# Optimization experiments

Measured on AMD Instinct MI355X. Metric: run time of the kernel, lower is better.

Reference implementation:

```python
import jax, jax.numpy as jnp
import numpy as np

C = 256
RED = 8
CR = C // RED  # 32
B, H, W = 4, 64, 64
EPS = 1e-5


def setup_inputs() -> dict:
    key = jax.random.key(0)
    ks = jax.random.split(key, 12)
    s = 0.05
    return {
        "x": jax.random.normal(ks[0], (B, C, H, W), dtype=jnp.float32),
        "Wq": jax.random.normal(ks[1], (CR, C), dtype=jnp.float32) * s,
        "bq": jax.random.normal(ks[2], (CR,), dtype=jnp.float32) * s,
        "Wk": jax.random.normal(ks[3], (CR, C), dtype=jnp.float32) * s,
        "bk": jax.random.normal(ks[4], (CR,), dtype=jnp.float32) * s,
        "Wv": jax.random.normal(ks[5], (C, C), dtype=jnp.float32) * s,
        "bv": jax.random.normal(ks[6], (C,), dtype=jnp.float32) * s,
        "Wo": jax.random.normal(ks[7], (C, C), dtype=jnp.float32) * s,
        "bo": jax.random.normal(ks[8], (C,), dtype=jnp.float32) * s,
        "gamma": jnp.ones((C,), dtype=jnp.float32),
        "beta": jnp.zeros((C,), dtype=jnp.float32),
        "running_mean": jax.random.normal(ks[9], (C,), dtype=jnp.float32) * s,
        "running_var": jax.random.uniform(ks[10], (C,), dtype=jnp.float32, minval=0.5, maxval=1.5),
    }


def reference(x, Wq, bq, Wk, bk, Wv, bv, Wo, bo, gamma, beta, running_mean, running_var):
    b, c, h, w = x.shape
    n = h * w
    scale = c ** (-0.5)  # use_scale=True: in_channels**-0.5
    xf = x.reshape(b, c, n)  # [B, C, N]
    # 1x1 convs == per-pixel channel matmuls
    q = jnp.einsum('oc,bcn->bon', Wq, xf) + bq[None, :, None]   # [B, CR, N]
    k = jnp.einsum('oc,bcn->bon', Wk, xf) + bk[None, :, None]   # [B, CR, N]
    v = jnp.einsum('oc,bcn->bon', Wv, xf) + bv[None, :, None]   # [B, C, N]
    # attention[b, q_pos, k_pos], softmax over key positions (dim=2)
    attn = jnp.einsum('bcq,bck->bqk', q, k) * scale             # [B, N, N]
    attn = jax.nn.softmax(attn, axis=2)
    # out[b, c, q_pos] = sum_k v[b, c, k] * attn[b, q_pos, k]
    out = jnp.einsum('bck,bqk->bcq', v, attn)                   # [B, C, N]
    out = jnp.einsum('oc,bcn->bon', Wo, out) + bo[None, :, None]
    # BatchNorm2d (inference: running stats)
    inv = gamma / jnp.sqrt(running_var + EPS)
    out = out * inv[None, :, None] + (beta - running_mean * inv)[None, :, None]
    out = out.reshape(b, c, h, w)
    return jax.nn.relu(out + x)
```

## Files before the change

### kernel.cpp

```cpp
#include <hip/hip_runtime.h>
#include <hip/hip_bf16.h>

typedef unsigned short u16;
typedef unsigned int u32;

#define B_ 4
#define C_ 256
#define N_ 4096

constexpr float C1 = 0.09016844005556021f;

typedef float f32x16 __attribute__((ext_vector_type(16)));
typedef short bf16x8 __attribute__((ext_vector_type(8)));
typedef u32 u32x4 __attribute__((ext_vector_type(4)));
typedef int i32x2 __attribute__((ext_vector_type(2)));

__device__ __forceinline__ u16 bf16r(float f) {
    union { float f; u32 u; } a; a.f = f;
    u32 u = a.u;
    u += 0x7fffu + ((u >> 16) & 1u);
    return (u16)(u >> 16);
}

__device__ __forceinline__ float bf2f(u16 h) {
    union { u32 u; float f; } a; a.u = ((u32)h) << 16; return a.f;
}

__device__ __forceinline__ u32 pk2(float a, float b) {
    __hip_bfloat162 h = __float22bfloat162_rn(make_float2(a, b));
    union { __hip_bfloat162 h; u32 u; } c; c.h = h;
    return c.u;
}

__device__ __forceinline__ u32 cvtpk(float lo, float hi) {
    u32 r;
    asm("v_cvt_pk_bf16_f32 %0, %1, %2" : "=v"(r) : "v"(lo), "v"(hi));
    return r;
}

__device__ __forceinline__ void swap32(u32 &a, u32 &b) {
#if __has_builtin(__builtin_amdgcn_permlane32_swap)
    i32x2 r = __builtin_amdgcn_permlane32_swap((int)a, (int)b, false, false);
    a = (u32)r.x; b = (u32)r.y;
#else
    u32 as = __shfl_xor(a, 32), bs = __shfl_xor(b, 32);
    int hi = (threadIdx.x & 32) ? 1 : 0;
    u32 na = hi ? bs : a;
    u32 nb = hi ? b : as;
    a = na; b = nb;
#endif
}

__device__ __forceinline__ bf16x8 ld8(const u16* p) {
    return *reinterpret_cast<const bf16x8*>(p);
}

__device__ __forceinline__ void gld_lds16(const u16* g, u16* lbase, int lane) {
#if __has_builtin(__builtin_amdgcn_global_load_lds)
    __builtin_amdgcn_global_load_lds(
        (const __attribute__((address_space(1))) void*)g,
        (__attribute__((address_space(3))) void*)lbase, 16, 0, 0);
#else
    *reinterpret_cast<bf16x8*>(lbase + lane * 8) = ld8(g);
#endif
}

__device__ __forceinline__ int crow(int r, int hi) { return (r & 3) + 8 * (r >> 2) + 4 * hi; }

__global__ __launch_bounds__(256) void prep(
    const float* __restrict__ Wq, const float* __restrict__ Wk,
    const float* __restrict__ Wv, const float* __restrict__ Wo,
    const float* __restrict__ bo, const float* __restrict__ gamma,
    const float* __restrict__ beta, const float* __restrict__ rm, const float* __restrict__ rv,
    u16* __restrict__ wqk, u16* __restrict__ wv_b, u16* __restrict__ wo_b,
    float* __restrict__ scale, float* __restrict__ shift)
{
    int i = blockIdx.x * 256 + threadIdx.x;
    if (i < 16384) {
        float w = (i < 8192) ? Wq[i] * C1 : Wk[i - 8192];
        wqk[i] = bf16r(w);
    } else if (i < 81920) {
        wv_b[i - 16384] = bf16r(Wv[i - 16384]);
    } else if (i < 147456) {
        wo_b[i - 81920] = bf16r(Wo[i - 81920]);
    } else if (i < 147712) {
        int o = i - 147456;
        float inv = gamma[o] * rsqrtf(rv[o] + 1e-5f);
        scale[o] = inv;
        shift[o] = beta[o] + (bo[o] - rm[o]) * inv;
    }
}

__global__ __launch_bounds__(512) void projf(
    const float* __restrict__ x, const u16* __restrict__ wqk, const u16* __restrict__ wv,
    const float* __restrict__ bq, const float* __restrict__ bk, const float* __restrict__ bv,
    u16* __restrict__ qkt, u16* __restrict__ vout)
{
    __shared__ u16 xt[64 * 256];
    int tid = threadIdx.x;
    int lane = tid & 63, wid = tid >> 6;
    int r31 = lane & 31, hi = lane >> 5;
    int b = blockIdx.y, n0 = blockIdx.x * 64;
    const float* xb = x + (size_t)b * C_ * N_ + n0;
#pragma unroll
    for (int i = 0; i < 16; ++i) {
        int c2 = i * 8 + wid;
        int n = lane;
        float a0 = xb[(size_t)(2 * c2) * N_ + n];
        float a1 = xb[(size_t)(2 * c2 + 1) * N_ + n];
        int slot = (c2 >> 2) ^ (n & 31);
        *reinterpret_cast<u32*>(&xt[n * 256 + slot * 8 + (c2 & 3) * 2]) = pk2(a0, a1);
    }
    __syncthreads();
    for (int i = 0; i < 3; ++i) {
        int t = wid + i * 8;
        if (t < 20) {
            bool isqk = (t < 4);
            int nb = isqk ? (t >> 1) * 32 : ((t - 4) & 1) * 32;
            int gb = isqk ? (t & 1) * 32 : ((t - 4) >> 1) * 32;
            const u16* grow = (isqk ? wqk : wv) + (size_t)(gb + r31) * C_ + hi * 8;
            f32x16 acc;
#pragma unroll
            for (int r = 0; r < 16; ++r) acc[r] = 0.f;
#pragma unroll
            for (int ks = 0; ks < 16; ++ks) {
                int slot = (2 * ks + hi) ^ r31;
                bf16x8 lf = ld8(&xt[(nb + r31) * 256 + slot * 8]);
                bf16x8 gf = ld8(grow + ks * 16);
                if (isqk) acc = __builtin_amdgcn_mfma_f32_32x32x16_bf16(lf, gf, acc, 0, 0, 0);
                else      acc = __builtin_amdgcn_mfma_f32_32x32x16_bf16(gf, lf, acc, 0, 0, 0);
            }
            if (isqk) {
                int o = gb + r31;
                float bias = (o < 32) ? bq[o] * C1 : bk[o - 32];
                u16* qrow = qkt + ((size_t)b * N_ + n0 + nb) * 64 + o;
#pragma unroll
                for (int r = 0; r < 16; ++r)
                    qrow[(size_t)crow(r, hi) * 64] = bf16r(acc[r] + bias);
            } else {
                u16* vb = vout + (size_t)b * C_ * N_ + n0 + nb + r31;
#pragma unroll
                for (int r = 0; r < 16; ++r) {
                    int c = gb + crow(r, hi);
                    vb[(size_t)c * N_] = bf16r(acc[r] + bv[c]);
                }
            }
        }
    }
}

__global__ __launch_bounds__(256, 2) void attn(
    const u16* __restrict__ qkt, const u16* __restrict__ v,
    u16* __restrict__ opart, float* __restrict__ lpart, int kts)
{
    __shared__ char smem[73728];
    u16* vt0 = (u16*)smem;
    u16* kt0 = (u16*)(smem + 65536);
    int tid = threadIdx.x;
    int lane = tid & 63, wid = tid >> 6;
    int r31 = lane & 31, hi = lane >> 5;

    int nwg = 32 * 4 * gridDim.z;
    int wgl = blockIdx.x + 32 * (blockIdx.y + 4 * blockIdx.z);
    int cpx = nwg >> 3;
    int swzid = (wgl & 7) * cpx + (wgl >> 3);
    int bx = swzid & 31;
    int by = (swzid >> 5) & 3;
    int bz = swzid >> 7;

    int b = by, zs = bz;
    int q0 = bx * 128 + wid * 32;
    const u16* qkb = qkt + (size_t)b * N_ * 64;
    const u16* vbase = v + (size_t)b * C_ * N_;

    int ks_row = tid >> 4;
    int ks_so = (tid & 15) ^ ks_row;
    int ks_k = ks_row * 4 + (ks_so >> 2);
    int ks_d8 = (ks_so & 3) * 8;

    int cpar8 = (r31 & 1) * 8;
    int vrow0 = r31 >> 1;
    int kr4 = r31 >> 2;
    int kk3 = (r31 & 3) * 4;

    bf16x8 qf0 = ld8(qkb + (size_t)(q0 + r31) * 64 + hi * 8);
    bf16x8 qf1 = ld8(qkb + (size_t)(q0 + r31) * 64 + 16 + hi * 8);

    f32x16 acc[8];
#pragma unroll
    for (int ct = 0; ct < 8; ++ct)
#pragma unroll
        for (int r = 0; r < 16; ++r) acc[ct][r] = 0.f;

    f32x16 z4;
#pragma unroll
    for (int r = 0; r < 16; ++r) z4[r] = 0.f;

    float l0 = 0.f, l1 = 0.f, l2 = 0.f, l3 = 0.f;
    int ktBeg = zs * kts, ktEnd = (zs + 1) * kts;

    auto stage = [&](int buf, int kt) {
        int k0 = kt * 64;
        gld_lds16(qkb + (size_t)(k0 + ks_k) * 64 + 32 + ks_d8,
                  kt0 + buf * 2048 + wid * 512, lane);
#pragma unroll
        for (int i = 0; i < 8; ++i) {
            int q = i * 256 + tid;
            int row2 = q >> 4;
            int so = (q & 15) ^ (row2 & 15);
            int c = 2 * row2 + (so >> 3);
            int kcol = (so & 7) * 8;
            gld_lds16(vbase + (size_t)c * N_ + k0 + kcol,
                      vt0 + buf * 16384 + (i * 256 + wid * 64) * 8, lane);
        }
    };

    int cur = 0;
    stage(cur, ktBeg);
    __syncthreads();

    for (int kt = ktBeg; kt < ktEnd; ++kt) {
        if (kt + 1 < ktEnd) stage(cur ^ 1, kt + 1);

        bf16x8 pfm[4];
#pragma unroll
        for (int ph = 0; ph < 2; ++ph) {
            int krow = ph * 8 + kr4;
            const u16* kbase = kt0 + cur * 2048 + krow * 128;
            bf16x8 kf0 = ld8(kbase + (((kk3 + hi) ^ krow) * 8));
            bf16x8 kf1 = ld8(kbase + (((kk3 + 2 + hi) ^ krow) * 8));
            f32x16 s = __builtin_amdgcn_mfma_f32_32x32x16_bf16(kf0, qf0, z4, 0, 0, 0);
            s = __builtin_amdgcn_mfma_f32_32x32x16_bf16(kf1, qf1, s, 0, 0, 0);
            float p[16];
#pragma unroll
            for (int r = 0; r < 16; ++r) p[r] = __builtin_amdgcn_exp2f(s[r]);
            l0 += (p[0] + p[1]) + (p[2] + p[3]);
            l1 += (p[4] + p[5]) + (p[6] + p[7]);
            l2 += (p[8] + p[9]) + (p[10] + p[11]);
            l3 += (p[12] + p[13]) + (p[14] + p[15]);
#pragma unroll
            for (int c16 = 0; c16 < 2; ++c16) {
                u32 w0 = cvtpk(p[8 * c16 + 0], p[8 * c16 + 1]);
                u32 w1 = cvtpk(p[8 * c16 + 2], p[8 * c16 + 3]);
                u32 w2 = cvtpk(p[8 * c16 + 4], p[8 * c16 + 5]);
                u32 w3 = cvtpk(p[8 * c16 + 6], p[8 * c16 + 7]);
                swap32(w0, w2);
                swap32(w1, w3);
                union { bf16x8 f8; u32 u[4]; } fu;
                fu.u[0] = w0; fu.u[1] = w1; fu.u[2] = w2; fu.u[3] = w3;
                pfm[ph * 2 + c16] = fu.f8;
            }
        }

        __builtin_amdgcn_s_setprio(1);
#pragma unroll
        for (int ct = 0; ct < 8; ++ct) {
            const u16* vb2 = vt0 + cur * 16384 + (vrow0 + 16 * ct) * 128;
#pragma unroll
            for (int c = 0; c < 4; ++c) {
                bf16x8 vf = ld8(vb2 + (((cpar8 + 2 * c + hi) ^ vrow0) * 8));
                acc[ct] = __builtin_amdgcn_mfma_f32_32x32x16_bf16(vf, pfm[c], acc[ct], 0, 0, 0);
            }
        }
        __builtin_amdgcn_s_setprio(0);

        __syncthreads();
        cur ^= 1;
    }

    float l_run = (l0 + l1) + (l2 + l3);
    l_run += __shfl_xor(l_run, 32);

    u16* dst = opart + ((size_t)(zs * B_ + b) * N_) * C_;
    if (hi == 0)
        lpart[((size_t)zs * B_ + b) * N_ + q0 + r31] = l_run;
    char* ep = smem + wid * 16896;
#pragma unroll
    for (int ct = 0; ct < 8; ++ct)
#pragma unroll
        for (int rp = 0; rp < 8; ++rp) {
            int r2 = 2 * rp;
            int c = (r2 & 3) + 8 * (r2 >> 2) + 4 * hi;
            int cpos = ct * 16 + (c >> 1);
            *reinterpret_cast<u32*>(ep + r31 * 528 + cpos * 4) =
                cvtpk(acc[ct][r2], acc[ct][r2 + 1]);
        }
    asm volatile("s_waitcnt lgkmcnt(0)" ::: "memory");
    __builtin_amdgcn_sched_barrier(0);
#pragma unroll
    for (int i = 0; i < 16; ++i) {
        int row = 2 * i + (lane >> 5);
        u32x4 w = *reinterpret_cast<const u32x4*>(ep + row * 528 + (lane & 31) * 16);
        *reinterpret_cast<u32x4*>(dst + (size_t)(q0 + row) * C_ + (lane & 31) * 8) = w;
    }
}

__global__ __launch_bounds__(512) void outprojf(
    const u16* __restrict__ opart, const float* __restrict__ lpart,
    const u16* __restrict__ wo, const float* __restrict__ scl, const float* __restrict__ shf,
    const float* __restrict__ x, float* __restrict__ out, int S)
{
    __shared__ u16 ot[64 * 256];
    __shared__ float linv[64];
    int tid = threadIdx.x;
    int lane = tid & 63, wid = tid >> 6;
    int r31 = lane & 31, hi = lane >> 5;
    int b = blockIdx.y, n0 = blockIdx.x * 64;
    if (tid < 64) {
        float l = 0.f;
        for (int s = 0; s < S; ++s) l += lpart[((size_t)s * B_ + b) * N_ + n0 + tid];
        linv[tid] = 1.f / l;
    }
    __syncthreads();
#pragma unroll
    for (int i = 0; i < 4; ++i) {
        int chunk = i * 512 + tid;
        int n = chunk >> 5, c8 = chunk & 31;
        float a[8];
#pragma unroll
        for (int j = 0; j < 8; ++j) a[j] = 0.f;
        for (int s = 0; s < S; ++s) {
            bf16x8 o = ld8(opart + (((size_t)s * B_ + b) * N_ + n0 + n) * C_ + c8 * 8);
#pragma unroll
            for (int j = 0; j < 8; ++j) a[j] += bf2f((u16)o[j]);
        }
        float li = linv[n];
        u32x4 w;
#pragma unroll
        for (int j = 0; j < 4; ++j) w[j] = pk2(a[2 * j] * li, a[2 * j + 1] * li);
        int sws = c8 ^ (n & 31);
        *reinterpret_cast<u32x4*>(&ot[n * 256 + sws * 8]) = w;
    }
    __syncthreads();
    int obs = wid * 32;
    const u16* arow = wo + (size_t)(obs + r31) * C_ + hi * 8;
    f32x16 acc0, acc1;
#pragma unroll
    for (int r = 0; r < 16; ++r) { acc0[r] = 0.f; acc1[r] = 0.f; }
#pragma unroll
    for (int ks = 0; ks < 16; ++ks) {
        bf16x8 af = ld8(arow + ks * 16);
        int slot = (2 * ks + hi) ^ r31;
        bf16x8 b0 = ld8(&ot[r31 * 256 + slot * 8]);
        bf16x8 b1 = ld8(&ot[(32 + r31) * 256 + slot * 8]);
        acc0 = __builtin_amdgcn_mfma_f32_32x32x16_bf16(af, b0, acc0, 0, 0, 0);
        acc1 = __builtin_amdgcn_mfma_f32_32x32x16_bf16(af, b1, acc1, 0, 0, 0);
    }
    const float* xb = x + (size_t)b * C_ * N_;
    float* op = out + (size_t)b * C_ * N_;
#pragma unroll
    for (int r = 0; r < 16; ++r) {
        int o = obs + crow(r, hi);
        float sc = scl[o], sh = shf[o];
        size_t base = (size_t)o * N_ + n0;
        float v0 = acc0[r] * sc + sh + xb[base + r31];
        op[base + r31] = fmaxf(v0, 0.f);
        float v1 = acc1[r] * sc + sh + xb[base + 32 + r31];
        op[base + 32 + r31] = fmaxf(v1, 0.f);
    }
}

extern "C" void kernel_launch(void* const* d_in, const int* in_sizes, int n_in,
                              void* d_out, int out_size, void* d_ws, size_t ws_size,
                              hipStream_t stream) {
    const float* x     = (const float*)d_in[0];
    const float* Wq    = (const float*)d_in[1];
    const float* bq    = (const float*)d_in[2];
    const float* Wk    = (const float*)d_in[3];
    const float* bk    = (const float*)d_in[4];
    const float* Wv    = (const float*)d_in[5];
    const float* bv    = (const float*)d_in[6];
    const float* Wo    = (const float*)d_in[7];
    const float* bo    = (const float*)d_in[8];
    const float* gamma = (const float*)d_in[9];
    const float* beta  = (const float*)d_in[10];
    const float* rmean = (const float*)d_in[11];
    const float* rvar  = (const float*)d_in[12];
    float* out = (float*)d_out;

    char* ws = (char*)d_ws;
    u16* vbuf = (u16*)(ws);
    u16* qkt  = (u16*)(ws + (size_t)(8u << 20));
    char* wsm = ws + (size_t)(10u << 20);
    u16* wqk  = (u16*)(wsm);
    u16* wv_b = (u16*)(wsm + 32768);
    u16* wo_b = (u16*)(wsm + 32768 + 131072);
    float* scl = (float*)(wsm + 32768 + 262144);
    float* shf = scl + 256;
    float* lpart = (float*)(ws + (size_t)(11u << 20));
    u16* opart = (u16*)(ws + (size_t)(12u << 20));

    size_t need4 = (size_t)(12u << 20) + 4 * (size_t)(8u << 20);
    size_t need2 = (size_t)(12u << 20) + 2 * (size_t)(8u << 20);
    int S = (ws_size >= need4) ? 4 : (ws_size >= need2) ? 2 : 1;

    prep<<<dim3(578), dim3(256), 0, stream>>>(Wq, Wk, Wv, Wo, bo, gamma, beta, rmean, rvar,
                                              wqk, wv_b, wo_b, scl, shf);
    projf<<<dim3(64, 4), dim3(512), 0, stream>>>(x, wqk, wv_b, bq, bk, bv, qkt, vbuf);
    attn<<<dim3(32, 4, S), dim3(256), 0, stream>>>(qkt, vbuf, opart, lpart, 64 / S);
    outprojf<<<dim3(64, 4), dim3(512), 0, stream>>>(opart, lpart, wo_b, scl, shf, x, out, S);
}
```

Baseline: 80.09 us.

## Software-pipeline QK softmax one tile ahead of PV with triple-buffered K

Restructures the attention main loop so the QK^T MFMA and exp2 work for tile t+1 runs before the PV MFMAs for tile t. K tiles are triple-buffered in LDS (which grows by 4 KB) and P fragments ping-pong between two register sets, while V stays double-buffered. The goal is to let the exp/convert VALU work overlap with the PV matrix work and hide its latency. In exchange, keeping two P fragment sets live and the larger LDS footprint raise register and LDS pressure, which could hurt occupancy at 2 blocks per CU.

New measurement: 176.6 us. +120.6%, slower.

```diff
diff --git a/kernel.cpp b/kernel.cpp
--- a/kernel.cpp
+++ b/kernel.cpp
@@ -153,7 +153,7 @@
     const u16* __restrict__ qkt, const u16* __restrict__ v,
     u16* __restrict__ opart, float* __restrict__ lpart, int kts)
 {
-    __shared__ char smem[73728];
+    __shared__ char smem[77824];
     u16* vt0 = (u16*)smem;
     u16* kt0 = (u16*)(smem + 65536);
     int tid = threadIdx.x;
@@ -199,10 +199,8 @@
     float l0 = 0.f, l1 = 0.f, l2 = 0.f, l3 = 0.f;
     int ktBeg = zs * kts, ktEnd = (zs + 1) * kts;
 
-    auto stage = [&](int buf, int kt) {
+    auto stageV = [&](int vs, int kt) {
         int k0 = kt * 64;
-        gld_lds16(qkb + (size_t)(k0 + ks_k) * 64 + 32 + ks_d8,
-                  kt0 + buf * 2048 + wid * 512, lane);
 #pragma unroll
         for (int i = 0; i < 8; ++i) {
             int q = i * 256 + tid;
@@ -211,22 +209,20 @@
             int c = 2 * row2 + (so >> 3);
             int kcol = (so & 7) * 8;
             gld_lds16(vbase + (size_t)c * N_ + k0 + kcol,
-                      vt0 + buf * 16384 + (i * 256 + wid * 64) * 8, lane);
+                      vt0 + vs * 16384 + (i * 256 + wid * 64) * 8, lane);
         }
     };
-
-    int cur = 0;
-    stage(cur, ktBeg);
-    __syncthreads();
-
-    for (int kt = ktBeg; kt < ktEnd; ++kt) {
-        if (kt + 1 < ktEnd) stage(cur ^ 1, kt + 1);
-
-        bf16x8 pfm[4];
+    auto stageK = [&](int ks, int kt) {
+        int k0 = kt * 64;
+        gld_lds16(qkb + (size_t)(k0 + ks_k) * 64 + 32 + ks_d8,
+                  kt0 + ks * 2048 + wid * 512, lane);
+    };
+
+    auto qksm = [&](int kslot, bf16x8* pf) {
 #pragma unroll
         for (int ph = 0; ph < 2; ++ph) {
             int krow = ph * 8 + kr4;
-            const u16* kbase = kt0 + cur * 2048 + krow * 128;
+            const u16* kbase = kt0 + kslot * 2048 + krow * 128;
             bf16x8 kf0 = ld8(kbase + (((kk3 + hi) ^ krow) * 8));
             bf16x8 kf1 = ld8(kbase + (((kk3 + 2 + hi) ^ krow) * 8));
             f32x16 s = __builtin_amdgcn_mfma_f32_32x32x16_bf16(kf0, qf0, z4, 0, 0, 0);
@@ -248,24 +244,46 @@
                 swap32(w1, w3);
                 union { bf16x8 f8; u32 u[4]; } fu;
                 fu.u[0] = w0; fu.u[1] = w1; fu.u[2] = w2; fu.u[3] = w3;
-                pfm[ph * 2 + c16] = fu.f8;
+                pf[ph * 2 + c16] = fu.f8;
             }
         }
-
+    };
+    auto pv = [&](int vs, const bf16x8* pf) {
         __builtin_amdgcn_s_setprio(1);
 #pragma unroll
         for (int ct = 0; ct < 8; ++ct) {
-            const u16* vb2 = vt0 + cur * 16384 + (vrow0 + 16 * ct) * 128;
+            const u16* vb2 = vt0 + vs * 16384 + (vrow0 + 16 * ct) * 128;
 #pragma unroll
             for (int c = 0; c < 4; ++c) {
                 bf16x8 vf = ld8(vb2 + (((cpar8 + 2 * c + hi) ^ vrow0) * 8));
-                acc[ct] = __builtin_amdgcn_mfma_f32_32x32x16_bf16(vf, pfm[c], acc[ct], 0, 0, 0);
+                acc[ct] = __builtin_amdgcn_mfma_f32_32x32x16_bf16(vf, pf[c], acc[ct], 0, 0, 0);
             }
         }
         __builtin_amdgcn_s_setprio(0);
-
+    };
+
+    bf16x8 pfA[4], pfB[4];
+    int vcur = 0;
+    stageV(0, ktBeg);
+    stageK(ktBeg % 3, ktBeg);
+    if (ktBeg + 1 < ktEnd) stageK((ktBeg + 1) % 3, ktBeg + 1);
+    __syncthreads();
+    qksm(ktBeg % 3, pfA);
+
+    for (int t = ktBeg; t < ktEnd; t += 2) {
+        if (t + 1 < ktEnd) stageV(vcur ^ 1, t + 1);
+        if (t + 2 < ktEnd) stageK((t + 2) % 3, t + 2);
+        if (t + 1 < ktEnd) qksm((t + 1) % 3, pfB);
+        pv(vcur, pfA);
         __syncthreads();
-        cur ^= 1;
+        vcur ^= 1;
+        if (t + 1 >= ktEnd) break;
+        if (t + 2 < ktEnd) stageV(vcur ^ 1, t + 2);
+        if (t + 3 < ktEnd) stageK((t + 3) % 3, t + 3);
+        if (t + 2 < ktEnd) qksm((t + 2) % 3, pfA);
+        pv(vcur, pfB);
+        __syncthreads();
+        vcur ^= 1;
     }
 
     float l_run = (l0 + l1) + (l2 + l3);
```
